# Performance work log

Measured on AMD Instinct MI355X. Metric: run time of the kernel, lower is better.

## Reference

```python
import jax, jax.numpy as jnp
import numpy as np

D_MODEL = 2048
NUM_EXPERTS = 64
TOP_K = 2


def setup_inputs() -> dict:
    key = jax.random.key(0)
    kx, kw, kb = jax.random.split(key, 3)
    x = jax.random.normal(kx, (4, 4096, D_MODEL), dtype=jnp.float32)
    # nn.Linear(d_model, num_experts): weight [num_experts, d_model], bias [num_experts]
    bound = 1.0 / np.sqrt(D_MODEL)
    W = jax.random.uniform(kw, (NUM_EXPERTS, D_MODEL), minval=-bound, maxval=bound, dtype=jnp.float32)
    b = jax.random.uniform(kb, (NUM_EXPERTS,), minval=-bound, maxval=bound, dtype=jnp.float32)
    return {"x": x, "W": W, "b": b}


def reference(x, W, b):
    # Eval mode: no noise injection (self.training is False).
    logits = jnp.einsum('bsd,ed->bse', x, W) + b          # [B, S, E]
    raw_weights = jax.nn.softmax(logits, axis=-1)          # [B, S, E]
    top_k_weights, top_k_indices = jax.lax.top_k(raw_weights, TOP_K)  # [B, S, K]
    normalized = top_k_weights / jnp.sum(top_k_weights, axis=-1, keepdims=True)
    return normalized, top_k_indices
```

## Files before the change

kernel.cpp:

```cpp
#include <hip/hip_runtime.h>
#include <math.h>

#define DM 2048
#define NEXP 64
#define NTOK 16384
#define NSLICE 4
#define KSL (DM / NSLICE)
#define KC 32
#define NCH (KSL / KC)
#define MBLK 64
#define NBLK1 ((NTOK / MBLK) * NSLICE)
#define NKG (DM / KC)
#define WFRAG_BYTES (NKG * 12 * 1024)
#define PART_BYTES (NSLICE * NEXP * NTOK * 4)

typedef __attribute__((ext_vector_type(8))) short short8;
typedef __attribute__((ext_vector_type(4))) short short4v;
typedef __attribute__((ext_vector_type(4))) float f32x4;

__device__ __forceinline__ void async16(void* lds, const void* g) {
  __builtin_amdgcn_global_load_lds(
      (const __attribute__((address_space(1))) unsigned int*)g,
      (__attribute__((address_space(3))) unsigned int*)lds, 16, 0, 0);
}

__device__ __forceinline__ void split3t(float f, unsigned short& h,
                                        unsigned short& m, unsigned short& l) {
  unsigned u = __float_as_uint(f);
  h = (unsigned short)(u >> 16);
  float f1 = f - __uint_as_float(u & 0xFFFF0000u);
  unsigned u1 = __float_as_uint(f1);
  m = (unsigned short)(u1 >> 16);
  float f2 = f1 - __uint_as_float(u1 & 0xFFFF0000u);
  l = (unsigned short)(__float_as_uint(f2) >> 16);
}

__device__ __forceinline__ void split8(const f32x4& a0, const f32x4& a1,
                                       short8& h, short8& m, short8& l) {
  float v[8] = {a0[0], a0[1], a0[2], a0[3], a1[0], a1[1], a1[2], a1[3]};
#pragma unroll
  for (int j = 0; j < 8; ++j) {
    unsigned short hh, mm, ll;
    split3t(v[j], hh, mm, ll);
    h[j] = (short)hh; m[j] = (short)mm; l[j] = (short)ll;
  }
}

__global__ void convw_kernel(const float* __restrict__ W,
                             unsigned short* __restrict__ wfrag) {
  const int kg = blockIdx.x;
  const int lane = threadIdx.x & 63;
  const int nt = threadIdx.x >> 6;
  const int e = nt * 16 + (lane & 15);
  const int kpos = kg * 32 + (lane >> 4) * 8;
  const f32x4* wp = (const f32x4*)(W + (size_t)e * DM + kpos);
  f32x4 w0 = wp[0], w1 = wp[1];
  short8 h, m, l;
  split8(w0, w1, h, m, l);
  size_t base = ((size_t)(kg * 12 + nt) * 64 + lane) * 8;
  *(short8*)(wfrag + base) = h;
  *(short8*)(wfrag + base + (size_t)4 * 64 * 8) = m;
  *(short8*)(wfrag + base + (size_t)8 * 64 * 8) = l;
}

__global__ __launch_bounds__(256, 4)
void router_gemm(const float* __restrict__ x,
                 const unsigned short* __restrict__ wfrag,
                 float* __restrict__ part) {
  const int lane = threadIdx.x & 63;
  const int wv = threadIdx.x >> 6;
  const int col = lane & 15;
  const int quad = lane >> 4;
  const int tg = blockIdx.x >> 2;
  const int s = blockIdx.x & 3;
  const int tok0 = tg * MBLK;

  __shared__ __align__(16) float xs[2][MBLK][KC];
  __shared__ __align__(16) unsigned short alim[3][4][64][8];

  const float* xsrc =
      x + (size_t)(tok0 + wv * 16 + (lane >> 3)) * DM + s * KSL + (lane & 7) * 4;

  auto stage = [&](int buf, int c) {
#pragma unroll
    for (int i = 0; i < 2; ++i)
      async16(&xs[buf][wv * 16 + i * 8][0], xsrc + (size_t)(i * 8) * DM + c * KC);
  };

  f32x4 acc[4];
#pragma unroll
  for (int mt = 0; mt < 4; ++mt) acc[mt] = (f32x4){0.f, 0.f, 0.f, 0.f};

  const unsigned short* bb = wfrag + (size_t)lane * 8;

  stage(0, 0);

  for (int c = 0; c < NCH; ++c) {
    const int cur = c & 1;
    const int kg = s * NCH + c;

    short8 B0 = *(const short8*)(bb + ((size_t)kg * 12 + 0 + wv) * 512);
    short8 B1 = *(const short8*)(bb + ((size_t)kg * 12 + 4 + wv) * 512);
    short8 B2 = *(const short8*)(bb + ((size_t)kg * 12 + 8 + wv) * 512);
    asm volatile("" ::: "memory");

    if (c + 1 < NCH) {
      stage(cur ^ 1, c + 1);
      asm volatile("s_waitcnt vmcnt(5)\n\ts_barrier" ::: "memory");
    } else {
      asm volatile("s_waitcnt vmcnt(3)\n\ts_barrier" ::: "memory");
    }

#pragma unroll
    for (int i = 0; i < 2; ++i) {
      const int row = wv * 16 + i * 8 + (lane >> 3);
      const int u = lane & 7;
      f32x4 v = *(const f32x4*)&xs[cur][row][u * 4];
      short4v h, m, l;
#pragma unroll
      for (int j = 0; j < 4; ++j) {
        unsigned short hh, mm, ll;
        split3t(v[j], hh, mm, ll);
        h[j] = (short)hh; m[j] = (short)mm; l[j] = (short)ll;
      }
      const int slot = (i * 8 + (lane >> 3)) + 16 * (u >> 1);
      const int half = (u & 1) * 4;
      *(short4v*)&alim[0][wv][slot][half] = h;
      *(short4v*)&alim[1][wv][slot][half] = m;
      *(short4v*)&alim[2][wv][slot][half] = l;
    }
    asm volatile("s_waitcnt lgkmcnt(0)\n\ts_barrier" ::: "memory");

#pragma unroll
    for (int mt = 0; mt < 4; ++mt) {
      short8 ah = *(const short8*)&alim[0][mt][lane][0];
      short8 am = *(const short8*)&alim[1][mt][lane][0];
      short8 al = *(const short8*)&alim[2][mt][lane][0];
      f32x4 cc = acc[mt];
      cc = __builtin_amdgcn_mfma_f32_16x16x32_bf16(ah, B0, cc, 0, 0, 0);
      cc = __builtin_amdgcn_mfma_f32_16x16x32_bf16(ah, B1, cc, 0, 0, 0);
      cc = __builtin_amdgcn_mfma_f32_16x16x32_bf16(am, B0, cc, 0, 0, 0);
      cc = __builtin_amdgcn_mfma_f32_16x16x32_bf16(ah, B2, cc, 0, 0, 0);
      cc = __builtin_amdgcn_mfma_f32_16x16x32_bf16(al, B0, cc, 0, 0, 0);
      cc = __builtin_amdgcn_mfma_f32_16x16x32_bf16(am, B1, cc, 0, 0, 0);
      acc[mt] = cc;
    }
  }

#pragma unroll
  for (int mt = 0; mt < 4; ++mt) {
    const size_t e = (size_t)(s * NEXP + wv * 16 + col);
    *(f32x4*)(part + e * NTOK + tok0 + mt * 16 + quad * 4) = acc[mt];
  }
}

__global__ __launch_bounds__(256, 4)
void router_reduce(const float* __restrict__ part,
                   const float* __restrict__ bias, float* __restrict__ out) {
  const int lane = threadIdx.x & 63;
  const int wv = threadIdx.x >> 6;
  const int q = lane >> 4;
  const int t = blockIdx.x * 64 + wv * 16 + (lane & 15);

  float v1 = -INFINITY, v2 = -INFINITY;
  int i1 = 0, i2 = 0;
#pragma unroll
  for (int e = 0; e < NEXP; ++e) {
    float p = part[(size_t)(q * NEXP + e) * NTOK + t];
    p += __shfl_xor(p, 16, 64);
    p += __shfl_xor(p, 32, 64);
    const float v = p + bias[e];
    const bool a = v > v1;
    const bool b = v > v2;
    const float nv2 = a ? v1 : (b ? v : v2);
    const int ni2 = a ? i1 : (b ? e : i2);
    v2 = nv2; i2 = ni2;
    i1 = a ? e : i1;
    v1 = a ? v : v1;
  }
  if (q == 0) {
    const float ex = expf(v2 - v1);
    const float den = 1.f + ex;
    *(float2*)(out + 2 * t) = make_float2(1.f / den, ex / den);
    *(float2*)(out + 2 * NTOK + 2 * t) = make_float2((float)i1, (float)i2);
  }
}

__global__ __launch_bounds__(512, 2)
void router_fb(const float* __restrict__ x, const float* __restrict__ W,
               const float* __restrict__ bias, float* __restrict__ out) {
  const int lane = threadIdx.x & 63;
  const int wv = threadIdx.x >> 6;
  const int col = lane & 15;
  const int quad = lane >> 4;
  const int tok0 = blockIdx.x * 32;
  const int k0 = wv * 256;

  __shared__ float part[8][32][68];

  f32x4 acc[2][4];
#pragma unroll
  for (int ms = 0; ms < 2; ++ms)
#pragma unroll
    for (int nt = 0; nt < 4; ++nt) acc[ms][nt] = (f32x4){0.f, 0.f, 0.f, 0.f};

  for (int ks = 0; ks < 8; ++ks) {
    const int k = k0 + ks * 32 + quad * 8;
    short8 ah[2], am2[2], al2[2];
#pragma unroll
    for (int ms = 0; ms < 2; ++ms) {
      const f32x4* ap = (const f32x4*)(x + (size_t)(tok0 + ms * 16 + col) * DM + k);
      f32x4 a0 = ap[0], a1 = ap[1];
      split8(a0, a1, ah[ms], am2[ms], al2[ms]);
    }
#pragma unroll
    for (int nt = 0; nt < 4; ++nt) {
      short8 bh, bm, bl;
      const f32x4* wp = (const f32x4*)(W + (size_t)(nt * 16 + col) * DM + k);
      f32x4 w0 = wp[0], w1 = wp[1];
      split8(w0, w1, bh, bm, bl);
#pragma unroll
      for (int ms = 0; ms < 2; ++ms) {
        f32x4 cc = acc[ms][nt];
        cc = __builtin_amdgcn_mfma_f32_16x16x32_bf16(ah[ms], bh, cc, 0, 0, 0);
        cc = __builtin_amdgcn_mfma_f32_16x16x32_bf16(ah[ms], bm, cc, 0, 0, 0);
        cc = __builtin_amdgcn_mfma_f32_16x16x32_bf16(am2[ms], bh, cc, 0, 0, 0);
        cc = __builtin_amdgcn_mfma_f32_16x16x32_bf16(ah[ms], bl, cc, 0, 0, 0);
        cc = __builtin_amdgcn_mfma_f32_16x16x32_bf16(al2[ms], bh, cc, 0, 0, 0);
        cc = __builtin_amdgcn_mfma_f32_16x16x32_bf16(am2[ms], bm, cc, 0, 0, 0);
        acc[ms][nt] = cc;
      }
    }
  }
#pragma unroll
  for (int ms = 0; ms < 2; ++ms)
#pragma unroll
    for (int nt = 0; nt < 4; ++nt)
#pragma unroll
      for (int r = 0; r < 4; ++r)
        part[wv][ms * 16 + quad * 4 + r][nt * 16 + col] = acc[ms][nt][r];
  __syncthreads();
  const float bl_ = bias[lane];
#pragma unroll
  for (int ti = 0; ti < 4; ++ti) {
    const int t = wv * 4 + ti;
    float v1 = bl_;
#pragma unroll
    for (int p = 0; p < 8; ++p) v1 += part[p][t][lane];
    int i1 = lane;
    float v2 = -INFINITY;
    int i2 = NEXP;
#pragma unroll
    for (int off = 32; off > 0; off >>= 1) {
      float ov1 = __shfl_xor(v1, off, 64);
      int   oi1 = __shfl_xor(i1, off, 64);
      float ov2 = __shfl_xor(v2, off, 64);
      int   oi2 = __shfl_xor(i2, off, 64);
      bool afirst = (v1 > ov1) || (v1 == ov1 && i1 < oi1);
      float w1v = afirst ? v1 : ov1;  int w1i = afirst ? i1 : oi1;
      float c1v = afirst ? v2 : ov2;  int c1i = afirst ? i2 : oi2;
      float c2v = afirst ? ov1 : v1;  int c2i = afirst ? oi1 : i1;
      bool sfirst = (c1v > c2v) || (c1v == c2v && c1i < c2i);
      v1 = w1v; i1 = w1i;
      v2 = sfirst ? c1v : c2v;
      i2 = sfirst ? c1i : c2i;
    }
    if (lane == 0) {
      const float ex = expf(v2 - v1);
      const float den = 1.f + ex;
      const int token = tok0 + t;
      *(float2*)(out + 2 * token) = make_float2(1.f / den, ex / den);
      *(float2*)(out + 2 * NTOK + 2 * token) =
          make_float2((float)i1, (float)i2);
    }
  }
}

extern "C" void kernel_launch(void* const* d_in, const int* in_sizes, int n_in,
                              void* d_out, int out_size, void* d_ws, size_t ws_size,
                              hipStream_t stream) {
  const float* x = (const float*)d_in[0];
  const float* W = (const float*)d_in[1];
  const float* b = (const float*)d_in[2];
  float* out = (float*)d_out;

  const size_t need = (size_t)WFRAG_BYTES + (size_t)PART_BYTES;
  if (ws_size >= need) {
    unsigned short* wfrag = (unsigned short*)d_ws;
    float* part = (float*)((char*)d_ws + WFRAG_BYTES);
    hipLaunchKernelGGL(convw_kernel, dim3(NKG), dim3(256), 0, stream, W, wfrag);
    hipLaunchKernelGGL(router_gemm, dim3(NBLK1), dim3(256), 0, stream,
                       x, wfrag, part);
    hipLaunchKernelGGL(router_reduce, dim3(NTOK / 64), dim3(256), 0, stream,
                       part, b, out);
  } else {
    hipLaunchKernelGGL(router_fb, dim3(NTOK / 32), dim3(512), 0, stream,
                       x, W, b, out);
  }
}
```

Measured before the change: 206.6 us.

## Load x directly into registers as MFMA A-fragments, drop LDS staging

```diff
diff --git a/kernel.cpp b/kernel.cpp
--- a/kernel.cpp
+++ b/kernel.cpp
@@ -18,12 +18,6 @@
 typedef __attribute__((ext_vector_type(4))) short short4v;
 typedef __attribute__((ext_vector_type(4))) float f32x4;
 
-__device__ __forceinline__ void async16(void* lds, const void* g) {
-  __builtin_amdgcn_global_load_lds(
-      (const __attribute__((address_space(1))) unsigned int*)g,
-      (__attribute__((address_space(3))) unsigned int*)lds, 16, 0, 0);
-}
-
 __device__ __forceinline__ void split3t(float f, unsigned short& h,
                                         unsigned short& m, unsigned short& l) {
   unsigned u = __float_as_uint(f);
@@ -74,83 +68,61 @@
   const int tg = blockIdx.x >> 2;
   const int s = blockIdx.x & 3;
   const int tok0 = tg * MBLK;
-
-  __shared__ __align__(16) float xs[2][MBLK][KC];
-  __shared__ __align__(16) unsigned short alim[3][4][64][8];
-
-  const float* xsrc =
-      x + (size_t)(tok0 + wv * 16 + (lane >> 3)) * DM + s * KSL + (lane & 7) * 4;
-
-  auto stage = [&](int buf, int c) {
-#pragma unroll
-    for (int i = 0; i < 2; ++i)
-      async16(&xs[buf][wv * 16 + i * 8][0], xsrc + (size_t)(i * 8) * DM + c * KC);
-  };
+  const int kg0 = s * NCH;
+
+  const float* xp =
+      x + (size_t)(tok0 + wv * 16 + col) * DM + s * KSL + quad * 8;
+  const unsigned short* bb = wfrag + (size_t)lane * 8;
 
   f32x4 acc[4];
 #pragma unroll
-  for (int mt = 0; mt < 4; ++mt) acc[mt] = (f32x4){0.f, 0.f, 0.f, 0.f};
-
-  const unsigned short* bb = wfrag + (size_t)lane * 8;
-
-  stage(0, 0);
-
+  for (int nt = 0; nt < 4; ++nt) acc[nt] = (f32x4){0.f, 0.f, 0.f, 0.f};
+
+  f32x4 pa0 = ((const f32x4*)xp)[0];
+  f32x4 pa1 = ((const f32x4*)xp)[1];
+  f32x4 qa0 = ((const f32x4*)(xp + KC))[0];
+  f32x4 qa1 = ((const f32x4*)(xp + KC))[1];
+
+  short8 Bh = *(const short8*)(bb + (size_t)(kg0 * 12 + 0) * 512);
+  short8 Bm = *(const short8*)(bb + (size_t)(kg0 * 12 + 4) * 512);
+  short8 Bl = *(const short8*)(bb + (size_t)(kg0 * 12 + 8) * 512);
+
+#pragma unroll
   for (int c = 0; c < NCH; ++c) {
-    const int cur = c & 1;
-    const int kg = s * NCH + c;
-
-    short8 B0 = *(const short8*)(bb + ((size_t)kg * 12 + 0 + wv) * 512);
-    short8 B1 = *(const short8*)(bb + ((size_t)kg * 12 + 4 + wv) * 512);
-    short8 B2 = *(const short8*)(bb + ((size_t)kg * 12 + 8 + wv) * 512);
-    asm volatile("" ::: "memory");
-
-    if (c + 1 < NCH) {
-      stage(cur ^ 1, c + 1);
-      asm volatile("s_waitcnt vmcnt(5)\n\ts_barrier" ::: "memory");
-    } else {
-      asm volatile("s_waitcnt vmcnt(3)\n\ts_barrier" ::: "memory");
-    }
-
-#pragma unroll
-    for (int i = 0; i < 2; ++i) {
-      const int row = wv * 16 + i * 8 + (lane >> 3);
-      const int u = lane & 7;
-      f32x4 v = *(const f32x4*)&xs[cur][row][u * 4];
-      short4v h, m, l;
-#pragma unroll
-      for (int j = 0; j < 4; ++j) {
-        unsigned short hh, mm, ll;
-        split3t(v[j], hh, mm, ll);
-        h[j] = (short)hh; m[j] = (short)mm; l[j] = (short)ll;
+    const int kg = kg0 + c;
+    short8 ah, am, al;
+    split8(pa0, pa1, ah, am, al);
+    pa0 = qa0; pa1 = qa1;
+    if (c + 2 < NCH) {
+      const float* xn = xp + (size_t)(c + 2) * KC;
+      qa0 = ((const f32x4*)xn)[0];
+      qa1 = ((const f32x4*)xn)[1];
+    }
+#pragma unroll
+    for (int nt = 0; nt < 4; ++nt) {
+      short8 bh = Bh, bm = Bm, bl = Bl;
+      const int nf = (nt < 3) ? (kg * 12 + nt + 1)
+                              : ((c + 1 < NCH) ? (kg + 1) * 12 : -1);
+      if (nf >= 0) {
+        Bh = *(const short8*)(bb + (size_t)(nf + 0) * 512);
+        Bm = *(const short8*)(bb + (size_t)(nf + 4) * 512);
+        Bl = *(const short8*)(bb + (size_t)(nf + 8) * 512);
       }
-      const int slot = (i * 8 + (lane >> 3)) + 16 * (u >> 1);
-      const int half = (u & 1) * 4;
-      *(short4v*)&alim[0][wv][slot][half] = h;
-      *(short4v*)&alim[1][wv][slot][half] = m;
-      *(short4v*)&alim[2][wv][slot][half] = l;
-    }
-    asm volatile("s_waitcnt lgkmcnt(0)\n\ts_barrier" ::: "memory");
-
-#pragma unroll
-    for (int mt = 0; mt < 4; ++mt) {
-      short8 ah = *(const short8*)&alim[0][mt][lane][0];
-      short8 am = *(const short8*)&alim[1][mt][lane][0];
-      short8 al = *(const short8*)&alim[2][mt][lane][0];
-      f32x4 cc = acc[mt];
-      cc = __builtin_amdgcn_mfma_f32_16x16x32_bf16(ah, B0, cc, 0, 0, 0);
-      cc = __builtin_amdgcn_mfma_f32_16x16x32_bf16(ah, B1, cc, 0, 0, 0);
-      cc = __builtin_amdgcn_mfma_f32_16x16x32_bf16(am, B0, cc, 0, 0, 0);
-      cc = __builtin_amdgcn_mfma_f32_16x16x32_bf16(ah, B2, cc, 0, 0, 0);
-      cc = __builtin_amdgcn_mfma_f32_16x16x32_bf16(al, B0, cc, 0, 0, 0);
-      cc = __builtin_amdgcn_mfma_f32_16x16x32_bf16(am, B1, cc, 0, 0, 0);
-      acc[mt] = cc;
-    }
-  }
-
-#pragma unroll
-  for (int mt = 0; mt < 4; ++mt) {
-    const size_t e = (size_t)(s * NEXP + wv * 16 + col);
-    *(f32x4*)(part + e * NTOK + tok0 + mt * 16 + quad * 4) = acc[mt];
+      f32x4 cc = acc[nt];
+      cc = __builtin_amdgcn_mfma_f32_16x16x32_bf16(ah, bh, cc, 0, 0, 0);
+      cc = __builtin_amdgcn_mfma_f32_16x16x32_bf16(ah, bm, cc, 0, 0, 0);
+      cc = __builtin_amdgcn_mfma_f32_16x16x32_bf16(am, bh, cc, 0, 0, 0);
+      cc = __builtin_amdgcn_mfma_f32_16x16x32_bf16(ah, bl, cc, 0, 0, 0);
+      cc = __builtin_amdgcn_mfma_f32_16x16x32_bf16(al, bh, cc, 0, 0, 0);
+      cc = __builtin_amdgcn_mfma_f32_16x16x32_bf16(am, bm, cc, 0, 0, 0);
+      acc[nt] = cc;
+    }
+  }
+
+#pragma unroll
+  for (int nt = 0; nt < 4; ++nt) {
+    const size_t e = (size_t)(s * NEXP + nt * 16 + col);
+    *(f32x4*)(part + e * NTOK + tok0 + wv * 16 + quad * 4) = acc[nt];
   }
 }
 
```

Measured after the change: 221.9 us. +7.4%, slower.
